# Optimization experiments

Measured on AMD Instinct MI355X. Metric: run time of the kernel, lower is better.

## Reference

```python
import jax, jax.numpy as jnp
import numpy as np

N_NODES = 50000
NEG_SLOPE = 0.2


def gat_layer(x, src, dst, w_src, w_dst, att_src, att_dst, bias):
    """Single-head PyG-style GATConv (bipartite weights, same x for src/dst)."""
    xs = x @ w_src                      # [N, C] messages (source projection)
    xd = x @ w_dst                      # [N, C] destination projection
    a_s = xs @ att_src                  # [N] per-node src attention logit
    a_d = xd @ att_dst                  # [N] per-node dst attention logit
    e = jax.nn.leaky_relu(a_s[src] + a_d[dst], NEG_SLOPE)   # [E]
    # segment softmax over edges grouped by destination node
    m = jax.ops.segment_max(e, dst, num_segments=N_NODES)    # [N]
    ex = jnp.exp(e - m[dst])
    denom = jax.ops.segment_sum(ex, dst, num_segments=N_NODES)  # [N]
    alpha = ex / denom[dst]             # [E]
    out = jax.ops.segment_sum(alpha[:, None] * xs[src], dst, num_segments=N_NODES)
    return out + bias


def setup_inputs() -> dict:
    key = jax.random.key(0)
    ks = jax.random.split(key, 12)
    d_in, hid, out = 256, 128, 128
    inv = lambda d: 1.0 / np.sqrt(d)
    x = jax.random.normal(ks[0], (N_NODES, d_in), dtype=jnp.float32)
    edge_index = jax.random.randint(ks[1], (2, 800000), 0, N_NODES, dtype=jnp.int32)
    return {
        "x": x,
        "edge_index": edge_index,
        "w1_src": jax.random.normal(ks[2], (d_in, hid), jnp.float32) * inv(d_in),
        "w1_dst": jax.random.normal(ks[3], (d_in, hid), jnp.float32) * inv(d_in),
        "att1_src": jax.random.normal(ks[4], (hid,), jnp.float32) * inv(hid),
        "att1_dst": jax.random.normal(ks[5], (hid,), jnp.float32) * inv(hid),
        "b1": jnp.zeros((hid,), jnp.float32),
        "w2_src": jax.random.normal(ks[6], (hid, out), jnp.float32) * inv(hid),
        "w2_dst": jax.random.normal(ks[7], (hid, out), jnp.float32) * inv(hid),
        "att2_src": jax.random.normal(ks[8], (out,), jnp.float32) * inv(out),
        "att2_dst": jax.random.normal(ks[9], (out,), jnp.float32) * inv(out),
        "b2": jnp.zeros((out,), jnp.float32),
    }


def reference(x, edge_index, w1_src, w1_dst, att1_src, att1_dst, b1,
              w2_src, w2_dst, att2_src, att2_dst, b2):
    # add self loops once (GATConv default add_self_loops=True)
    loop = jnp.arange(N_NODES, dtype=edge_index.dtype)
    src = jnp.concatenate([edge_index[0], loop])
    dst = jnp.concatenate([edge_index[1], loop])
    h = gat_layer(x, src, dst, w1_src, w1_dst, att1_src, att1_dst, b1)
    h = jax.nn.relu(h)
    return gat_layer(h, src, dst, w2_src, w2_dst, att2_src, att2_dst, b2)
```

## Files before the change

### kernel.cpp

```cpp
#include <hip/hip_runtime.h>

#define NN 50000
#define MAXD 64
#define NEG_SLOPE 0.2f

typedef _Float16 half8 __attribute__((ext_vector_type(8)));
typedef _Float16 half2v __attribute__((ext_vector_type(2)));
typedef float floatx4 __attribute__((ext_vector_type(4)));


__global__ __launch_bounds__(256) void prep_kernel(
    const int* __restrict__ src, const int* __restrict__ dst,
    int* cnt, int* seg, int e, int G_SCAT,
    const float* __restrict__ w1s, const float* __restrict__ a1s,
    const float* __restrict__ w1d, const float* __restrict__ a1d,
    const float* __restrict__ w2s, const float* __restrict__ a2s,
    const float* __restrict__ w2d, const float* __restrict__ a2d,
    float* u1, float* v1, float* u2, float* v2, int din,
    const float* __restrict__ x, _Float16* __restrict__ xh, int n8) {
  int bid = blockIdx.x, tid = threadIdx.x;
  if (bid < G_SCAT) {
    int i0 = (bid * 256 + tid) * 8;
    int total = e + NN;
#pragma unroll
    for (int j = 0; j < 8; ++j) {
      int i = i0 + j;
      if (i < total) {
        int d, s;
        if (i < e) { d = dst[i]; s = src[i]; }
        else       { d = i - e;  s = d; }
        int r = atomicAdd(&cnt[d], 1);
        if (r < MAXD) seg[(size_t)d * MAXD + r] = s;
      }
    }
  } else if (bid < G_SCAT + 4) {
    int b = bid - G_SCAT;
    const float *w, *a;
    float* o;
    int d;
    if (b == 0) { w = w1s; a = a1s; o = u1; d = din; }
    else if (b == 1) { w = w1d; a = a1d; o = v1; d = din; }
    else if (b == 2) { w = w2s; a = a2s; o = u2; d = 128; }
    else { w = w2d; a = a2d; o = v2; d = 128; }
    if (tid < d) {
      float s = 0.f;
      for (int j = 0; j < 128; ++j) s += w[tid * 128 + j] * a[j];
      o[tid] = s;
    }
  } else {
    int i = (bid - G_SCAT - 4) * 256 + tid;
    if (i >= n8) return;
    const float4* p = reinterpret_cast<const float4*>(x) + i * 2;
    float4 v0 = p[0], v1 = p[1];
    half8 h = {(_Float16)v0.x, (_Float16)v0.y, (_Float16)v0.z, (_Float16)v0.w,
               (_Float16)v1.x, (_Float16)v1.y, (_Float16)v1.z, (_Float16)v1.w};
    *reinterpret_cast<half8*>(xh + (size_t)i * 8) = h;
  }
}


template <int K>
__global__ __launch_bounds__(256) void fused_kernel(
    const _Float16* __restrict__ A, const float* __restrict__ B,
    _Float16* __restrict__ C, int M, int G_GEMM,
    const int* __restrict__ cnt, int* seg, int G_SORT,
    const _Float16* __restrict__ xin, const float* __restrict__ u,
    const float* __restrict__ v, float* a_s, float* a_d, int din) {
  constexpr int KP = 72;
  __shared__ _Float16 Bt[128 * KP];
  int bid = blockIdx.x, tid = threadIdx.x;
  if (bid < G_GEMM) {
    __builtin_amdgcn_s_setprio(1);
    int lane = tid & 63, wave = tid >> 6;
    int row_base = bid * 64 + wave * 16;
    int lr = lane & 15, lk = lane >> 4;
    floatx4 acc[8];
#pragma unroll
    for (int q = 0; q < 8; ++q) acc[q] = {0.f, 0.f, 0.f, 0.f};
    for (int kc = 0; kc < K; kc += 64) {
      for (int idx = tid; idx < 128 * 64; idx += 256) {
        int k = idx >> 7, c = idx & 127;
        Bt[c * KP + k] = (_Float16)B[(size_t)(kc + k) * 128 + c];
      }
      __syncthreads();
#pragma unroll
      for (int k0 = 0; k0 < 64; k0 += 32) {
        int row = row_base + lr;
        half8 a = {0, 0, 0, 0, 0, 0, 0, 0};
        if (row < M) a = *reinterpret_cast<const half8*>(&A[(size_t)row * K + kc + k0 + lk * 8]);
        half8 b[8];
#pragma unroll
        for (int q = 0; q < 8; ++q)
          b[q] = *reinterpret_cast<const half8*>(&Bt[(q * 16 + lr) * KP + k0 + lk * 8]);
#pragma unroll
        for (int q = 0; q < 8; ++q)
          acc[q] = __builtin_amdgcn_mfma_f32_16x16x32_f16(a, b[q], acc[q], 0, 0, 0);
      }
      __syncthreads();
    }
#pragma unroll
    for (int q = 0; q < 8; ++q)
#pragma unroll
      for (int r = 0; r < 4; ++r) {
        int row = row_base + lk * 4 + r;
        if (row < M) C[(size_t)row * 128 + q * 16 + lr] = (_Float16)acc[q][r];
      }
    __builtin_amdgcn_s_setprio(0);
  } else if (bid < G_GEMM + G_SORT) {
    int wid = (bid - G_GEMM) * 4 + (tid >> 6);
    int lane = tid & 63;
    if (wid < NN) {
      int L = cnt[wid];
      L = L < MAXD ? L : MAXD;
      if (L > 1) {
        int* srow = seg + (size_t)wid * MAXD;
        int v = (lane < L) ? srow[lane] : 0x7fffffff;
#pragma unroll
        for (int k = 2; k <= 64; k <<= 1) {
#pragma unroll
          for (int j = k >> 1; j > 0; j >>= 1) {
            int other = __shfl_xor(v, j);
            bool dir = ((lane & k) == 0);
            bool lower = ((lane & j) == 0);
            int mn = v < other ? v : other;
            int mx = v < other ? other : v;
            v = (dir == lower) ? mn : mx;
          }
        }
        if (lane < L) srow[lane] = v;
      }
    }
  } else {
    int lbid = bid - G_GEMM - G_SORT;
    int wid = lbid * 4 + (tid >> 6);
    int lane = tid & 63;
    if (wid >= NN) return;
    float s1 = 0.f, s2 = 0.f;
    const half2v* xr = reinterpret_cast<const half2v*>(&xin[(size_t)wid * din]);
    for (int i = lane; i < din / 2; i += 64) {
      half2v xv = xr[i];
      float x0 = (float)xv[0], x1 = (float)xv[1];
      s1 += x0 * u[2 * i] + x1 * u[2 * i + 1];
      s2 += x0 * v[2 * i] + x1 * v[2 * i + 1];
    }
#pragma unroll
    for (int off = 32; off; off >>= 1) {
      s1 += __shfl_xor(s1, off);
      s2 += __shfl_xor(s2, off);
    }
    if (lane == 0) { a_s[wid] = s1; a_d[wid] = s2; }
  }
}

template <int LAYER>
__global__ __launch_bounds__(256) void agg_kernel(const int* __restrict__ cnt,
                                                  const int* __restrict__ seg,
                                                  const float* __restrict__ a_s,
                                                  const float* __restrict__ a_d,
                                                  const _Float16* __restrict__ xs,
                                                  const float* __restrict__ bias,
                                                  void* __restrict__ outp, int n) {
  int wid = (blockIdx.x * blockDim.x + threadIdx.x) >> 6;
  int lane = threadIdx.x & 63;
  if (wid >= n) return;
  int g = lane >> 3, lr = lane & 7;
  int L = cnt[wid];
  L = L < MAXD ? L : MAXD;
  const int* srow = seg + (size_t)wid * MAXD;
  float ad = a_d[wid];

  float denom = 0.f;
  float acc[16];
#pragma unroll
  for (int j = 0; j < 16; ++j) acc[j] = 0.f;

  int i = g;
  int s_cur = (i < L) ? srow[i] : -1;
  int i2 = i + 8;
  int s_next = (i2 < L) ? srow[i2] : -1;
  half8 v_cur0, v_cur1;
  float as_cur = 0.f;
  if (s_cur >= 0) {
    const _Float16* pr = &xs[(size_t)s_cur * 128 + lr * 16];
    v_cur0 = *reinterpret_cast<const half8*>(pr);
    v_cur1 = *reinterpret_cast<const half8*>(pr + 8);
    as_cur = a_s[s_cur];
  }
  while (s_cur >= 0) {
    half8 v_nx0, v_nx1;
    float as_nx = 0.f;
    if (s_next >= 0) {
      const _Float16* pr = &xs[(size_t)s_next * 128 + lr * 16];
      v_nx0 = *reinterpret_cast<const half8*>(pr);
      v_nx1 = *reinterpret_cast<const half8*>(pr + 8);
      as_nx = a_s[s_next];
    }
    int i3 = i2 + 8;
    int s_nx2 = (i3 < L) ? srow[i3] : -1;

    float e = as_cur + ad;
    e = e > 0.f ? e : NEG_SLOPE * e;
    float w = __expf(e);
    denom += w;
#pragma unroll
    for (int j = 0; j < 8; ++j) {
      acc[j] += w * (float)v_cur0[j];
      acc[8 + j] += w * (float)v_cur1[j];
    }
    s_cur = s_next; v_cur0 = v_nx0; v_cur1 = v_nx1; as_cur = as_nx;
    s_next = s_nx2; i2 = i3;
  }
  denom += __shfl_xor(denom, 8);
  denom += __shfl_xor(denom, 16);
  denom += __shfl_xor(denom, 32);
#pragma unroll
  for (int j = 0; j < 16; ++j) {
    acc[j] += __shfl_xor(acc[j], 8);
    acc[j] += __shfl_xor(acc[j], 16);
    acc[j] += __shfl_xor(acc[j], 32);
  }
  if (g == 0) {
    float inv = 1.0f / denom;
    float o[16];
#pragma unroll
    for (int j = 0; j < 16; ++j) o[j] = acc[j] * inv + bias[lr * 16 + j];
    if (LAYER == 1) {
      half8 h0, h1;
#pragma unroll
      for (int j = 0; j < 8; ++j) {
        h0[j] = (_Float16)fmaxf(o[j], 0.f);
        h1[j] = (_Float16)fmaxf(o[8 + j], 0.f);
      }
      _Float16* op = &((_Float16*)outp)[(size_t)wid * 128 + lr * 16];
      *reinterpret_cast<half8*>(op) = h0;
      *reinterpret_cast<half8*>(op + 8) = h1;
    } else {
      float* op = &((float*)outp)[(size_t)wid * 128 + lr * 16];
#pragma unroll
      for (int q = 0; q < 4; ++q) {
        float4 f = make_float4(o[q * 4], o[q * 4 + 1], o[q * 4 + 2], o[q * 4 + 3]);
        *reinterpret_cast<float4*>(op + q * 4) = f;
      }
    }
  }
}

extern "C" void kernel_launch(void* const* d_in, const int* in_sizes, int n_in,
                              void* d_out, int out_size, void* d_ws, size_t ws_size,
                              hipStream_t stream) {
  const float* x        = (const float*)d_in[0];
  const int*   eidx     = (const int*)d_in[1];
  const float* w1_src   = (const float*)d_in[2];
  const float* w1_dst   = (const float*)d_in[3];
  const float* att1_src = (const float*)d_in[4];
  const float* att1_dst = (const float*)d_in[5];
  const float* b1       = (const float*)d_in[6];
  const float* w2_src   = (const float*)d_in[7];
  const float* w2_dst   = (const float*)d_in[8];
  const float* att2_src = (const float*)d_in[9];
  const float* att2_dst = (const float*)d_in[10];
  const float* b2       = (const float*)d_in[11];

  const int E = in_sizes[1] / 2;
  const int DIN = in_sizes[0] / NN;
  const int* src = eidx;
  const int* dst = eidx + E;

  _Float16* x_h = (_Float16*)d_out;
  _Float16* h_h = (_Float16*)d_out;
  float*    out = (float*)d_out;

  char* ws = (char*)d_ws;
  size_t off = 0;
  auto alloc = [&](size_t bytes) -> void* {
    void* p = ws + off;
    off = (off + bytes + 255) & ~(size_t)255;
    return p;
  };
  _Float16* xs_h = (_Float16*)alloc((size_t)NN * 128 * sizeof(_Float16));
  float* a_s     = (float*)alloc((size_t)NN * sizeof(float));
  float* a_d     = (float*)alloc((size_t)NN * sizeof(float));
  int*   cnt     = (int*)alloc((size_t)NN * sizeof(int));
  int*   seg     = (int*)alloc((size_t)NN * MAXD * sizeof(int));
  float* u1      = (float*)alloc(256 * sizeof(float));
  float* v1      = (float*)alloc(256 * sizeof(float));
  float* u2      = (float*)alloc(256 * sizeof(float));
  float* v2      = (float*)alloc(256 * sizeof(float));

  const int G_SCAT = ((E + NN) / 8 + 255) / 256;
  const int G_CVT  = (NN * DIN / 8 + 255) / 256;
  const int G_GEMM = (NN + 63) / 64;
  const int G_SORT = (NN + 3) / 4;
  const int G_LOG  = (NN + 3) / 4;
  const int wave_blocks = (NN * 64 + 255) / 256;

  hipMemsetAsync(cnt, 0, NN * sizeof(int), stream);

  prep_kernel<<<G_SCAT + 4 + G_CVT, 256, 0, stream>>>(
      src, dst, cnt, seg, E, G_SCAT,
      w1_src, att1_src, w1_dst, att1_dst, w2_src, att2_src, w2_dst, att2_dst,
      u1, v1, u2, v2, DIN, x, x_h, NN * DIN / 8);

  fused_kernel<256><<<G_GEMM + G_SORT + G_LOG, 256, 0, stream>>>(
      x_h, w1_src, xs_h, NN, G_GEMM,
      cnt, seg, G_SORT,
      x_h, u1, v1, a_s, a_d, DIN);

  agg_kernel<1><<<wave_blocks, 256, 0, stream>>>(cnt, seg, a_s, a_d, xs_h, b1, h_h, NN);

  fused_kernel<128><<<G_GEMM + 0 + G_LOG, 256, 0, stream>>>(
      h_h, w2_src, xs_h, NN, G_GEMM,
      cnt, seg, 0,
      h_h, u2, v2, a_s, a_d, 128);

  agg_kernel<2><<<wave_blocks, 256, 0, stream>>>(cnt, seg, a_s, a_d, xs_h, b2, out, NN);
}
```

Before: 179.0 us.

## Fuse fp32-to-fp16 conversion into layer-1 GEMM and restructure kernel grouping

```diff
diff --git a/kernel.cpp b/kernel.cpp
--- a/kernel.cpp
+++ b/kernel.cpp
@@ -9,15 +9,17 @@
 typedef float floatx4 __attribute__((ext_vector_type(4)));
 
 
-__global__ __launch_bounds__(256) void prep_kernel(
+__global__ __launch_bounds__(256) void mega_kernel(
     const int* __restrict__ src, const int* __restrict__ dst,
     int* cnt, int* seg, int e, int G_SCAT,
     const float* __restrict__ w1s, const float* __restrict__ a1s,
     const float* __restrict__ w1d, const float* __restrict__ a1d,
     const float* __restrict__ w2s, const float* __restrict__ a2s,
     const float* __restrict__ w2d, const float* __restrict__ a2d,
-    float* u1, float* v1, float* u2, float* v2, int din,
-    const float* __restrict__ x, _Float16* __restrict__ xh, int n8) {
+    float* u1, float* v1, float* u2, float* v2,
+    const float* __restrict__ x, _Float16* __restrict__ C, int M, int G_GEMM) {
+  constexpr int K = 256, KP = 72;
+  __shared__ _Float16 Bt[128 * KP];
   int bid = blockIdx.x, tid = threadIdx.x;
   if (bid < G_SCAT) {
     int i0 = (bid * 256 + tid) * 8;
@@ -38,8 +40,8 @@
     const float *w, *a;
     float* o;
     int d;
-    if (b == 0) { w = w1s; a = a1s; o = u1; d = din; }
-    else if (b == 1) { w = w1d; a = a1d; o = v1; d = din; }
+    if (b == 0) { w = w1s; a = a1s; o = u1; d = K; }
+    else if (b == 1) { w = w1d; a = a1d; o = v1; d = K; }
     else if (b == 2) { w = w2s; a = a2s; o = u2; d = 128; }
     else { w = w2d; a = a2d; o = v2; d = 128; }
     if (tid < d) {
@@ -48,25 +50,106 @@
       o[tid] = s;
     }
   } else {
-    int i = (bid - G_SCAT - 4) * 256 + tid;
-    if (i >= n8) return;
-    const float4* p = reinterpret_cast<const float4*>(x) + i * 2;
-    float4 v0 = p[0], v1 = p[1];
-    half8 h = {(_Float16)v0.x, (_Float16)v0.y, (_Float16)v0.z, (_Float16)v0.w,
-               (_Float16)v1.x, (_Float16)v1.y, (_Float16)v1.z, (_Float16)v1.w};
-    *reinterpret_cast<half8*>(xh + (size_t)i * 8) = h;
-  }
-}
-
-
-template <int K>
-__global__ __launch_bounds__(256) void fused_kernel(
+    __builtin_amdgcn_s_setprio(1);
+    int gb = bid - G_SCAT - 4;
+    int lane = tid & 63, wave = tid >> 6;
+    int row_base = gb * 64 + wave * 16;
+    int lr = lane & 15, lk = lane >> 4;
+    floatx4 acc[8];
+#pragma unroll
+    for (int q = 0; q < 8; ++q) acc[q] = {0.f, 0.f, 0.f, 0.f};
+    for (int kc = 0; kc < K; kc += 64) {
+      for (int idx = tid; idx < 128 * 64; idx += 256) {
+        int k = idx >> 7, c = idx & 127;
+        Bt[c * KP + k] = (_Float16)w1s[(size_t)(kc + k) * 128 + c];
+      }
+      __syncthreads();
+#pragma unroll
+      for (int k0 = 0; k0 < 64; k0 += 32) {
+        int row = row_base + lr;
+        half8 a = {0, 0, 0, 0, 0, 0, 0, 0};
+        if (row < M) {
+          const float* ap = x + (size_t)row * K + kc + k0 + lk * 8;
+          float4 f0 = *reinterpret_cast<const float4*>(ap);
+          float4 f1 = *reinterpret_cast<const float4*>(ap + 4);
+          a = half8{(_Float16)f0.x, (_Float16)f0.y, (_Float16)f0.z, (_Float16)f0.w,
+                    (_Float16)f1.x, (_Float16)f1.y, (_Float16)f1.z, (_Float16)f1.w};
+        }
+        half8 b[8];
+#pragma unroll
+        for (int q = 0; q < 8; ++q)
+          b[q] = *reinterpret_cast<const half8*>(&Bt[(q * 16 + lr) * KP + k0 + lk * 8]);
+#pragma unroll
+        for (int q = 0; q < 8; ++q)
+          acc[q] = __builtin_amdgcn_mfma_f32_16x16x32_f16(a, b[q], acc[q], 0, 0, 0);
+      }
+      __syncthreads();
+    }
+#pragma unroll
+    for (int q = 0; q < 8; ++q)
+#pragma unroll
+      for (int r = 0; r < 4; ++r) {
+        int row = row_base + lk * 4 + r;
+        if (row < M) C[(size_t)row * 128 + q * 16 + lr] = (_Float16)acc[q][r];
+      }
+    __builtin_amdgcn_s_setprio(0);
+  }
+}
+
+__global__ __launch_bounds__(256) void ls_kernel(
+    const int* __restrict__ cnt, int* seg, int G_SORT,
+    const float* __restrict__ x, const float* __restrict__ u,
+    const float* __restrict__ v, float* a_s, float* a_d) {
+  int bid = blockIdx.x, tid = threadIdx.x;
+  if (bid < G_SORT) {
+    int wid = bid * 4 + (tid >> 6);
+    int lane = tid & 63;
+    if (wid < NN) {
+      int L = cnt[wid];
+      L = L < MAXD ? L : MAXD;
+      if (L > 1) {
+        int* srow = seg + (size_t)wid * MAXD;
+        int v2_ = (lane < L) ? srow[lane] : 0x7fffffff;
+#pragma unroll
+        for (int k = 2; k <= 64; k <<= 1) {
+#pragma unroll
+          for (int j = k >> 1; j > 0; j >>= 1) {
+            int other = __shfl_xor(v2_, j);
+            bool dir = ((lane & k) == 0);
+            bool lower = ((lane & j) == 0);
+            int mn = v2_ < other ? v2_ : other;
+            int mx = v2_ < other ? other : v2_;
+            v2_ = (dir == lower) ? mn : mx;
+          }
+        }
+        if (lane < L) srow[lane] = v2_;
+      }
+    }
+  } else {
+    int wid = (bid - G_SORT) * 4 + (tid >> 6);
+    int lane = tid & 63;
+    if (wid >= NN) return;
+    const float* xr = x + (size_t)wid * 256 + lane * 4;
+    float4 xv = *reinterpret_cast<const float4*>(xr);
+    float4 uu = *reinterpret_cast<const float4*>(u + lane * 4);
+    float4 vv = *reinterpret_cast<const float4*>(v + lane * 4);
+    float s1 = xv.x * uu.x + xv.y * uu.y + xv.z * uu.z + xv.w * uu.w;
+    float s2 = xv.x * vv.x + xv.y * vv.y + xv.z * vv.z + xv.w * vv.w;
+#pragma unroll
+    for (int off = 32; off; off >>= 1) {
+      s1 += __shfl_xor(s1, off);
+      s2 += __shfl_xor(s2, off);
+    }
+    if (lane == 0) { a_s[wid] = s1; a_d[wid] = s2; }
+  }
+}
+
+__global__ __launch_bounds__(256) void fused2_kernel(
     const _Float16* __restrict__ A, const float* __restrict__ B,
     _Float16* __restrict__ C, int M, int G_GEMM,
-    const int* __restrict__ cnt, int* seg, int G_SORT,
     const _Float16* __restrict__ xin, const float* __restrict__ u,
-    const float* __restrict__ v, float* a_s, float* a_d, int din) {
-  constexpr int KP = 72;
+    const float* __restrict__ v, float* a_s, float* a_d) {
+  constexpr int K = 128, KP = 72;
   __shared__ _Float16 Bt[128 * KP];
   int bid = blockIdx.x, tid = threadIdx.x;
   if (bid < G_GEMM) {
@@ -106,42 +189,18 @@
         if (row < M) C[(size_t)row * 128 + q * 16 + lr] = (_Float16)acc[q][r];
       }
     __builtin_amdgcn_s_setprio(0);
-  } else if (bid < G_GEMM + G_SORT) {
+  } else {
     int wid = (bid - G_GEMM) * 4 + (tid >> 6);
-    int lane = tid & 63;
-    if (wid < NN) {
-      int L = cnt[wid];
-      L = L < MAXD ? L : MAXD;
-      if (L > 1) {
-        int* srow = seg + (size_t)wid * MAXD;
-        int v = (lane < L) ? srow[lane] : 0x7fffffff;
-#pragma unroll
-        for (int k = 2; k <= 64; k <<= 1) {
-#pragma unroll
-          for (int j = k >> 1; j > 0; j >>= 1) {
-            int other = __shfl_xor(v, j);
-            bool dir = ((lane & k) == 0);
-            bool lower = ((lane & j) == 0);
-            int mn = v < other ? v : other;
-            int mx = v < other ? other : v;
-            v = (dir == lower) ? mn : mx;
-          }
-        }
-        if (lane < L) srow[lane] = v;
-      }
-    }
-  } else {
-    int lbid = bid - G_GEMM - G_SORT;
-    int wid = lbid * 4 + (tid >> 6);
     int lane = tid & 63;
     if (wid >= NN) return;
     float s1 = 0.f, s2 = 0.f;
-    const half2v* xr = reinterpret_cast<const half2v*>(&xin[(size_t)wid * din]);
-    for (int i = lane; i < din / 2; i += 64) {
+    const half2v* xr = reinterpret_cast<const half2v*>(&xin[(size_t)wid * 128]);
+    {
+      int i = lane;
       half2v xv = xr[i];
       float x0 = (float)xv[0], x1 = (float)xv[1];
-      s1 += x0 * u[2 * i] + x1 * u[2 * i + 1];
-      s2 += x0 * v[2 * i] + x1 * v[2 * i + 1];
+      s1 = x0 * u[2 * i] + x1 * u[2 * i + 1];
+      s2 = x0 * v[2 * i] + x1 * v[2 * i + 1];
     }
 #pragma unroll
     for (int off = 32; off; off >>= 1) {
@@ -262,11 +321,9 @@
   const float* b2       = (const float*)d_in[11];
 
   const int E = in_sizes[1] / 2;
-  const int DIN = in_sizes[0] / NN;
   const int* src = eidx;
   const int* dst = eidx + E;
 
-  _Float16* x_h = (_Float16*)d_out;
   _Float16* h_h = (_Float16*)d_out;
   float*    out = (float*)d_out;
 
@@ -288,7 +345,6 @@
   float* v2      = (float*)alloc(256 * sizeof(float));
 
   const int G_SCAT = ((E + NN) / 8 + 255) / 256;
-  const int G_CVT  = (NN * DIN / 8 + 255) / 256;
   const int G_GEMM = (NN + 63) / 64;
   const int G_SORT = (NN + 3) / 4;
   const int G_LOG  = (NN + 3) / 4;
@@ -296,22 +352,17 @@
 
   hipMemsetAsync(cnt, 0, NN * sizeof(int), stream);
 
-  prep_kernel<<<G_SCAT + 4 + G_CVT, 256, 0, stream>>>(
+  mega_kernel<<<G_SCAT + 4 + G_GEMM, 256, 0, stream>>>(
       src, dst, cnt, seg, E, G_SCAT,
       w1_src, att1_src, w1_dst, att1_dst, w2_src, att2_src, w2_dst, att2_dst,
-      u1, v1, u2, v2, DIN, x, x_h, NN * DIN / 8);
-
-  fused_kernel<256><<<G_GEMM + G_SORT + G_LOG, 256, 0, stream>>>(
-      x_h, w1_src, xs_h, NN, G_GEMM,
-      cnt, seg, G_SORT,
-      x_h, u1, v1, a_s, a_d, DIN);
+      u1, v1, u2, v2, x, xs_h, NN, G_GEMM);
+
+  ls_kernel<<<G_SORT + G_LOG, 256, 0, stream>>>(cnt, seg, G_SORT, x, u1, v1, a_s, a_d);
 
   agg_kernel<1><<<wave_blocks, 256, 0, stream>>>(cnt, seg, a_s, a_d, xs_h, b1, h_h, NN);
 
-  fused_kernel<128><<<G_GEMM + 0 + G_LOG, 256, 0, stream>>>(
-      h_h, w2_src, xs_h, NN, G_GEMM,
-      cnt, seg, 0,
-      h_h, u2, v2, a_s, a_d, 128);
+  fused2_kernel<<<G_GEMM + G_LOG, 256, 0, stream>>>(
+      h_h, w2_src, xs_h, NN, G_GEMM, h_h, u2, v2, a_s, a_d);
 
   agg_kernel<2><<<wave_blocks, 256, 0, stream>>>(cnt, seg, a_s, a_d, xs_h, b2, out, NN);
 }
```

Result: faster. 165.9 us (-7.3%).
